# Kernel optimization log

Hardware: AMD Instinct MI355X
Metric: run time of the kernel (lower is better)

Reference implementation:

```python
import jax, jax.numpy as jnp
import numpy as np


def setup_inputs() -> dict:
    key = jax.random.key(0)
    ks = jax.random.split(key, 7)
    C, IC, H, W, B = 512, 256, 64, 64, 8
    N = H * W
    return {
        "x": jax.random.normal(ks[0], (B, C, H, W), dtype=jnp.float32),
        "w_phi": jax.random.normal(ks[1], (IC, C), dtype=jnp.float32) * 0.02,
        "w_theta": jax.random.normal(ks[2], (IC, C), dtype=jnp.float32) * 0.02,
        "w_g": jax.random.normal(ks[3], (IC, C), dtype=jnp.float32) * 0.02,
        "w_mask": jax.random.normal(ks[4], (C, IC), dtype=jnp.float32) * 0.02,
        "pos_embedding": jax.random.normal(ks[5], (1, N, N), dtype=jnp.float32),
        "pos_embedding_decoder": jax.random.normal(ks[6], (1, IC, H, W), dtype=jnp.float32),
    }


def reference(x, w_phi, w_theta, w_g, w_mask, pos_embedding, pos_embedding_decoder):
    b, c, h, w = x.shape
    n = h * w
    xf = x.reshape(b, c, n)  # [b, c, n]
    # 1x1 convs as channel matmuls
    phi = jnp.einsum('oc,bcn->bon', w_phi, xf)      # [b, ic, n]
    theta = jnp.einsum('oc,bcn->bon', w_theta, xf)  # [b, ic, n]
    g = jnp.einsum('oc,bcn->bon', w_g, xf) + pos_embedding_decoder.reshape(1, -1, n)
    g = jnp.swapaxes(g, 1, 2)  # [b, n, ic]
    # attention logits: theta^T @ phi -> [b, n_theta, n_phi], plus learned pos bias
    attn = jnp.einsum('bci,bcj->bij', theta, phi) + pos_embedding
    # NOTE: original softmax is over dim=1 (the theta/query axis), non-standard
    attn = jax.nn.softmax(attn, axis=1)
    y = jnp.einsum('bij,bjc->bic', attn, g)  # [b, n, ic]
    y = jnp.swapaxes(y, 1, 2).reshape(b, -1, n)  # [b, ic, n]
    mask = jnp.einsum('oc,bcn->bon', w_mask, y).reshape(b, c, h, w)
    return mask + x
```

## Files before the change

kernel.cpp:

```cpp
#include <hip/hip_runtime.h>

typedef short bf8 __attribute__((ext_vector_type(8)));
typedef float f32x4 __attribute__((ext_vector_type(4)));
typedef unsigned short us4 __attribute__((ext_vector_type(4)));
typedef unsigned short us8 __attribute__((ext_vector_type(8)));

#define DEVI __device__ __forceinline__

constexpr int NB = 8, NC = 512, NIC = 256, NS = 4096;

constexpr size_t OFF_XT  = 0;
constexpr size_t OFF_TP  = 33554432;
constexpr size_t OFF_POS = 67108864;
constexpr size_t OFF_G   = 100663296;
constexpr size_t OFF_G2  = 117440512;
constexpr size_t OFF_Y   = 134217728;
constexpr size_t OFF_WTP = 150994944;
constexpr size_t OFF_WG  = 151519232;
constexpr size_t OFF_WM  = 151781376;
constexpr size_t OFF_SP  = 152043520;

DEVI unsigned short f2bf(float f){
  unsigned u = __float_as_uint(f);
  u += 0x7fffu + ((u >> 16) & 1u);
  return (unsigned short)(u >> 16);
}
DEVI float bf2f(unsigned short b){ return __uint_as_float(((unsigned)b) << 16); }

DEVI void gld16(const void* g, void* l){
  __builtin_amdgcn_global_load_lds((const __attribute__((address_space(1))) unsigned int*)g,
                                   (__attribute__((address_space(3))) unsigned int*)l, 16, 0, 0);
}

DEVI void stage128x32(unsigned short* dst, const unsigned short* src, int ld, int wid, int lane){
#pragma unroll
  for (int r = 0; r < 2; ++r){
    int instr = wid + r * 4;
    int row = instr * 16 + (lane >> 2);
    gld16(src + (size_t)row * ld + (lane & 3) * 8, dst + instr * 512);
  }
}

DEVI void zero44(f32x4 (&a)[4][4]){
  f32x4 z = {0.f, 0.f, 0.f, 0.f};
#pragma unroll
  for (int i = 0; i < 4; ++i)
#pragma unroll
    for (int j = 0; j < 4; ++j) a[i][j] = z;
}

template<int NK>
DEVI void gemm128(const unsigned short* Ag, int lda, const unsigned short* Bg, int ldb,
                  unsigned short (&Ab)[2][4096], unsigned short (&Bb)[2][4096],
                  f32x4 (&acc)[4][4], int wid, int lane)
{
  const int wr = wid >> 1, wc = wid & 1;
  stage128x32(Ab[0], Ag, lda, wid, lane);
  stage128x32(Bb[0], Bg, ldb, wid, lane);
  __syncthreads();
  for (int kk = 0; kk < NK; ++kk){
    int cur = kk & 1;
    if (kk + 1 < NK){
      stage128x32(Ab[cur ^ 1], Ag + (kk + 1) * 32, lda, wid, lane);
      stage128x32(Bb[cur ^ 1], Bg + (kk + 1) * 32, ldb, wid, lane);
    }
    bf8 a[4], b[4];
#pragma unroll
    for (int f = 0; f < 4; ++f){
      a[f] = *(const bf8*)&Ab[cur][(wr * 64 + f * 16 + (lane & 15)) * 32 + (lane >> 4) * 8];
      b[f] = *(const bf8*)&Bb[cur][(wc * 64 + f * 16 + (lane & 15)) * 32 + (lane >> 4) * 8];
    }
#pragma unroll
    for (int i = 0; i < 4; ++i)
#pragma unroll
      for (int j = 0; j < 4; ++j)
        acc[i][j] = __builtin_amdgcn_mfma_f32_16x16x32_bf16(a[i], b[j], acc[i][j], 0, 0, 0);
    __syncthreads();
  }
}


__global__ void k_prep(const float* wphi, const float* wtheta, const float* wgf, const float* wmf,
                       unsigned short* wtp, unsigned short* wgb, unsigned short* wmb){
  int idx = (blockIdx.x * 256 + threadIdx.x) * 4;
  const float* src; unsigned short* dst;
  if (idx < 131072)      { src = wphi + idx;            dst = wtp + idx; }
  else if (idx < 262144) { src = wtheta + (idx - 131072); dst = wtp + idx; }
  else if (idx < 393216) { src = wgf + (idx - 262144);  dst = wgb + (idx - 262144); }
  else                   { src = wmf + (idx - 393216);  dst = wmb + (idx - 393216); }
  f32x4 v = *(const f32x4*)src;
  us4 o;
#pragma unroll
  for (int r = 0; r < 4; ++r) o[r] = f2bf(v[r]);
  *(us4*)dst = o;
}

__global__ void k_pos(const float* pos, unsigned short* posb){
  size_t base = ((size_t)blockIdx.x * 256 + threadIdx.x) * 8;
  f32x4 v0 = *(const f32x4*)&pos[base];
  f32x4 v1 = *(const f32x4*)&pos[base + 4];
  us8 o;
#pragma unroll
  for (int r = 0; r < 4; ++r){ o[r] = f2bf(v0[r]); o[r + 4] = f2bf(v1[r]); }
  *(us8*)&posb[base] = o;
}

__global__ void k_xt(const float* x, unsigned short* xT){
  int b = blockIdx.z, ct = blockIdx.y, nt = blockIdx.x;
  __shared__ float t[64][65];
  int tid = threadIdx.x;
  int c0 = ct * 64, n0 = nt * 64;
  const float* xp = x + (size_t)b * NC * NS;
#pragma unroll
  for (int it = 0; it < 16; ++it){
    int idx = it * 256 + tid; int r = idx >> 6, cc = idx & 63;
    t[r][cc] = xp[(size_t)(c0 + r) * NS + n0 + cc];
  }
  __syncthreads();
  unsigned short* xo = xT + (size_t)b * NS * NC;
#pragma unroll
  for (int it = 0; it < 16; ++it){
    int idx = it * 256 + tid; int r = idx >> 6, cc = idx & 63;
    xo[(size_t)(n0 + r) * NC + c0 + cc] = f2bf(t[cc][r]);
  }
}


__global__ __launch_bounds__(256, 2) void k_tp(const unsigned short* wtp, const unsigned short* xT,
                                               unsigned short* tp){
  int b = blockIdx.z, ot = blockIdx.y, nt = blockIdx.x;
  int tid = threadIdx.x, wid = tid >> 6, lane = tid & 63, wr = wid >> 1, wc = wid & 1;
  __shared__ unsigned short Ab[2][4096], Bb[2][4096];
  f32x4 acc[4][4]; zero44(acc);
  gemm128<16>(wtp + (size_t)(ot * 128) * 512, 512,
              xT + ((size_t)b * NS + nt * 128) * 512, 512, Ab, Bb, acc, wid, lane);
  unsigned short* out = tp + (size_t)b * NS * 512;
#pragma unroll
  for (int fr = 0; fr < 4; ++fr)
#pragma unroll
    for (int fc = 0; fc < 4; ++fc){
      int o0 = ot * 128 + wr * 64 + fr * 16 + ((lane >> 4) << 2);
      int n  = nt * 128 + wc * 64 + fc * 16 + (lane & 15);
      us4 v;
#pragma unroll
      for (int r = 0; r < 4; ++r) v[r] = f2bf(acc[fr][fc][r]);
      *(us4*)&out[(size_t)n * 512 + o0] = v;
    }
}

__global__ __launch_bounds__(256, 2) void k_g(const unsigned short* xT, const unsigned short* wgb,
                                              const float* pdec, unsigned short* gb){
  int b = blockIdx.z, ot = blockIdx.y, nt = blockIdx.x;
  int tid = threadIdx.x, wid = tid >> 6, lane = tid & 63, wr = wid >> 1, wc = wid & 1;
  __shared__ unsigned short Ab[2][4096], Bb[2][4096];
  f32x4 acc[4][4]; zero44(acc);
  gemm128<16>(xT + ((size_t)b * NS + nt * 128) * 512, 512,
              wgb + (size_t)(ot * 128) * 512, 512, Ab, Bb, acc, wid, lane);
#pragma unroll
  for (int fr = 0; fr < 4; ++fr)
#pragma unroll
    for (int fc = 0; fc < 4; ++fc){
      int n0 = nt * 128 + wr * 64 + fr * 16 + ((lane >> 4) << 2);
      int o  = ot * 128 + wc * 64 + fc * 16 + (lane & 15);
      f32x4 pd = *(const f32x4*)&pdec[(size_t)o * NS + n0];
      us4 v;
#pragma unroll
      for (int r = 0; r < 4; ++r) v[r] = f2bf(acc[fr][fc][r] + pd[r]);
      *(us4*)&gb[((size_t)b * NIC + o) * NS + n0] = v;
    }
}

__global__ __launch_bounds__(256, 2) void k_stats(const unsigned short* tp, const unsigned short* posb,
                                                  float* sp){
  int b = blockIdx.z, ih = blockIdx.y, jt = blockIdx.x;
  int tid = threadIdx.x, wid = tid >> 6, lane = tid & 63, wr = wid >> 1, wc = wid & 1;
  __shared__ unsigned short Ab[2][4096], Bb[2][4096];
  __shared__ float sred[2][2][64];
  float sacc[4][4];
#pragma unroll
  for (int i = 0; i < 4; ++i)
#pragma unroll
    for (int j = 0; j < 4; ++j) sacc[i][j] = 0.f;
  const unsigned short* tpb = tp + (size_t)b * NS * 512;
  const unsigned short* Ag = tpb + (size_t)(jt * 128) * 512;
  for (int it8 = 0; it8 < 8; ++it8){
    int i0 = (ih * 8 + it8) * 128;
    const unsigned short* Bg = tpb + (size_t)i0 * 512 + 256;
    f32x4 acc[4][4]; zero44(acc);
    gemm128<8>(Ag, 512, Bg, 512, Ab, Bb, acc, wid, lane);
#pragma unroll
    for (int fr = 0; fr < 4; ++fr)
#pragma unroll
      for (int fc = 0; fc < 4; ++fc){
        int ig  = i0 + wc * 64 + fc * 16 + (lane & 15);
        int jg0 = jt * 128 + wr * 64 + fr * 16 + ((lane >> 4) << 2);
        us4 pv = *(const us4*)&posb[(size_t)ig * NS + jg0];
#pragma unroll
        for (int r = 0; r < 4; ++r)
          sacc[fr][r] += __expf(acc[fr][fc][r] + bf2f(pv[r]));
      }
  }
#pragma unroll
  for (int m = 1; m <= 8; m <<= 1)
#pragma unroll
    for (int fr = 0; fr < 4; ++fr)
#pragma unroll
      for (int r = 0; r < 4; ++r)
        sacc[fr][r] += __shfl_xor(sacc[fr][r], m, 64);
  if ((lane & 15) == 0){
#pragma unroll
    for (int fr = 0; fr < 4; ++fr)
#pragma unroll
      for (int r = 0; r < 4; ++r)
        sred[wr][wc][fr * 16 + ((lane >> 4) << 2) + r] = sacc[fr][r];
  }
  __syncthreads();
  if (tid < 128){
    int jl = tid;
    sp[((size_t)b * 4 + ih) * NS + jt * 128 + jl] = sred[jl >> 6][0][jl & 63] + sred[jl >> 6][1][jl & 63];
  }
}

__global__ void k_sg(const unsigned short* gb, const float* sp, unsigned short* g2){
  size_t base = ((size_t)blockIdx.x * 256 + threadIdx.x) * 8;
  int b = (int)(base / ((size_t)NIC * NS));
  int j0 = (int)(base % NS);
  const float* spb = sp + (size_t)b * 4 * NS + j0;
  us8 gv = *(const us8*)&gb[base];
  us8 o;
#pragma unroll
  for (int r = 0; r < 8; ++r){
    float s = spb[r] + spb[NS + r] + spb[2 * NS + r] + spb[3 * NS + r];
    o[r] = f2bf(bf2f(gv[r]) / s);
  }
  *(us8*)&g2[base] = o;
}

__global__ __launch_bounds__(256, 2) void k_y(const unsigned short* tp, const unsigned short* posb,
                                              const unsigned short* g2, unsigned short* yb){
  int b = blockIdx.y, i0 = blockIdx.x * 64;
  int tid = threadIdx.x, wid = tid >> 6, lane = tid & 63;
  __shared__ unsigned short Th[64 * 264];
  __shared__ unsigned short Aph[2][4096];
  __shared__ unsigned short El[64 * 136];
  const unsigned short* tpb = tp + (size_t)b * NS * 512;
#pragma unroll
  for (int t = 0; t < 8; ++t){
    int cid = t * 256 + tid; int row = cid >> 5, ch = cid & 31;
    *(us8*)&Th[row * 264 + ch * 8] = *(const us8*)&tpb[(size_t)(i0 + row) * 512 + 256 + ch * 8];
  }
  f32x4 yacc[4][4]; zero44(yacc);
  __syncthreads();
  const unsigned short* g2b = g2 + (size_t)b * NIC * NS;
  for (int jt = 0; jt < 32; ++jt){
    int j0 = jt * 128;
    f32x4 lacc[2][4];
    {
      f32x4 z = {0.f, 0.f, 0.f, 0.f};
#pragma unroll
      for (int i = 0; i < 2; ++i)
#pragma unroll
        for (int j = 0; j < 4; ++j) lacc[i][j] = z;
    }
    stage128x32(Aph[0], tpb + (size_t)j0 * 512, 512, wid, lane);
    __syncthreads();
    for (int kk = 0; kk < 8; ++kk){
      int cur = kk & 1;
      if (kk < 7) stage128x32(Aph[cur ^ 1], tpb + (size_t)j0 * 512 + (kk + 1) * 32, 512, wid, lane);
      bf8 a[2], bbf[4];
#pragma unroll
      for (int f = 0; f < 2; ++f)
        a[f] = *(const bf8*)&Aph[cur][(wid * 32 + f * 16 + (lane & 15)) * 32 + (lane >> 4) * 8];
#pragma unroll
      for (int f = 0; f < 4; ++f)
        bbf[f] = *(const bf8*)&Th[(f * 16 + (lane & 15)) * 264 + kk * 32 + (lane >> 4) * 8];
#pragma unroll
      for (int i = 0; i < 2; ++i)
#pragma unroll
        for (int j = 0; j < 4; ++j)
          lacc[i][j] = __builtin_amdgcn_mfma_f32_16x16x32_bf16(a[i], bbf[j], lacc[i][j], 0, 0, 0);
      __syncthreads();
    }
#pragma unroll
    for (int fr = 0; fr < 2; ++fr)
#pragma unroll
      for (int fc = 0; fc < 4; ++fc){
        int il  = fc * 16 + (lane & 15);
        int jl0 = wid * 32 + fr * 16 + ((lane >> 4) << 2);
        us4 pv = *(const us4*)&posb[(size_t)(i0 + il) * NS + j0 + jl0];
        us4 ev;
#pragma unroll
        for (int r = 0; r < 4; ++r)
          ev[r] = f2bf(__expf(lacc[fr][fc][r] + bf2f(pv[r])));
        *(us4*)&El[il * 136 + jl0] = ev;
      }
    __syncthreads();
#pragma unroll
    for (int jk = 0; jk < 4; ++jk){
      bf8 eb[4];
#pragma unroll
      for (int f = 0; f < 4; ++f)
        eb[f] = *(const bf8*)&El[(f * 16 + (lane & 15)) * 136 + jk * 32 + (lane >> 4) * 8];
#pragma unroll
      for (int cf = 0; cf < 4; ++cf){
        int c = wid * 64 + cf * 16 + (lane & 15);
        bf8 ga = *(const bf8*)&g2b[(size_t)c * NS + j0 + jk * 32 + (lane >> 4) * 8];
#pragma unroll
        for (int f = 0; f < 4; ++f)
          yacc[cf][f] = __builtin_amdgcn_mfma_f32_16x16x32_bf16(ga, eb[f], yacc[cf][f], 0, 0, 0);
      }
    }
    __syncthreads();
  }
  unsigned short* yo = yb + (size_t)b * NS * NIC;
#pragma unroll
  for (int cf = 0; cf < 4; ++cf)
#pragma unroll
    for (int f = 0; f < 4; ++f){
      int c0 = wid * 64 + cf * 16 + ((lane >> 4) << 2);
      int ig = i0 + f * 16 + (lane & 15);
      us4 v;
#pragma unroll
      for (int r = 0; r < 4; ++r) v[r] = f2bf(yacc[cf][f][r]);
      *(us4*)&yo[(size_t)ig * NIC + c0] = v;
    }
}

__global__ __launch_bounds__(256, 2) void k_out(const unsigned short* yb, const unsigned short* wmb,
                                                const float* xg, float* outg){
  int b = blockIdx.z, cot = blockIdx.y, nt = blockIdx.x;
  int tid = threadIdx.x, wid = tid >> 6, lane = tid & 63, wr = wid >> 1, wc = wid & 1;
  __shared__ unsigned short Ab[2][4096], Bb[2][4096];
  f32x4 acc[4][4]; zero44(acc);
  gemm128<8>(yb + ((size_t)b * NS + nt * 128) * 256, 256,
             wmb + (size_t)(cot * 128) * 256, 256, Ab, Bb, acc, wid, lane);
#pragma unroll
  for (int fr = 0; fr < 4; ++fr)
#pragma unroll
    for (int fc = 0; fc < 4; ++fc){
      int n0 = nt * 128 + wr * 64 + fr * 16 + ((lane >> 4) << 2);
      int co = cot * 128 + wc * 64 + fc * 16 + (lane & 15);
      f32x4 xv = *(const f32x4*)&xg[((size_t)b * NC + co) * NS + n0];
      f32x4 ov = acc[fr][fc] + xv;
      *(f32x4*)&outg[((size_t)b * NC + co) * NS + n0] = ov;
    }
}

extern "C" void kernel_launch(void* const* d_in, const int* in_sizes, int n_in,
                              void* d_out, int out_size, void* d_ws, size_t ws_size,
                              hipStream_t stream){
  const float* x      = (const float*)d_in[0];
  const float* wphi   = (const float*)d_in[1];
  const float* wtheta = (const float*)d_in[2];
  const float* wgf    = (const float*)d_in[3];
  const float* wmf    = (const float*)d_in[4];
  const float* pos    = (const float*)d_in[5];
  const float* pdec   = (const float*)d_in[6];
  float* outg = (float*)d_out;
  char* ws = (char*)d_ws;
  unsigned short* xT   = (unsigned short*)(ws + OFF_XT);
  unsigned short* tp   = (unsigned short*)(ws + OFF_TP);
  unsigned short* posb = (unsigned short*)(ws + OFF_POS);
  unsigned short* gb   = (unsigned short*)(ws + OFF_G);
  unsigned short* g2   = (unsigned short*)(ws + OFF_G2);
  unsigned short* yb   = (unsigned short*)(ws + OFF_Y);
  unsigned short* wtp  = (unsigned short*)(ws + OFF_WTP);
  unsigned short* wgb  = (unsigned short*)(ws + OFF_WG);
  unsigned short* wmb  = (unsigned short*)(ws + OFF_WM);
  float* sp = (float*)(ws + OFF_SP);

  k_prep<<<512, 256, 0, stream>>>(wphi, wtheta, wgf, wmf, wtp, wgb, wmb);
  k_pos<<<8192, 256, 0, stream>>>(pos, posb);
  k_xt<<<dim3(64, 8, 8), 256, 0, stream>>>(x, xT);
  k_tp<<<dim3(32, 4, 8), 256, 0, stream>>>(wtp, xT, tp);
  k_g<<<dim3(32, 2, 8), 256, 0, stream>>>(xT, wgb, pdec, gb);
  k_stats<<<dim3(32, 4, 8), 256, 0, stream>>>(tp, posb, sp);
  k_sg<<<4096, 256, 0, stream>>>(gb, sp, g2);
  k_y<<<dim3(64, 8), 256, 0, stream>>>(tp, posb, g2, yb);
  k_out<<<dim3(32, 4, 8), 256, 0, stream>>>(yb, wmb, x, outg);
}
```

Before: 583.2 us.

## Fold softmax normalization into attention kernel and use 8-wave blocks

Replaces the pass that rescales all of g by column sums with a tiny kernel computing reciprocal sums, applied to exp values inside k_y. k_y now uses 512 threads, with waves split 4x2 over j and i, so each wave holds a smaller accumulator tile. It also raises wave priority during the PV MFMA phase and drops the trailing barrier. This removes one full read and write of g and should improve latency hiding, but each block stages more per wave and the barrier removal may race on El between iterations.

```diff
diff --git a/kernel.cpp b/kernel.cpp
--- a/kernel.cpp
+++ b/kernel.cpp
@@ -13,7 +13,7 @@
 constexpr size_t OFF_TP  = 33554432;
 constexpr size_t OFF_POS = 67108864;
 constexpr size_t OFF_G   = 100663296;
-constexpr size_t OFF_G2  = 117440512;
+constexpr size_t OFF_RS  = 117440512;
 constexpr size_t OFF_Y   = 134217728;
 constexpr size_t OFF_WTP = 150994944;
 constexpr size_t OFF_WG  = 151519232;
@@ -39,6 +39,11 @@
     int row = instr * 16 + (lane >> 2);
     gld16(src + (size_t)row * ld + (lane & 3) * 8, dst + instr * 512);
   }
+}
+
+DEVI void stageA8(unsigned short* dst, const unsigned short* src, int ld, int wid, int lane){
+  int row = wid * 16 + (lane >> 2);
+  gld16(src + (size_t)row * ld + (lane & 3) * 8, dst + wid * 512);
 }
 
 DEVI void zero44(f32x4 (&a)[4][4]){
@@ -221,104 +226,108 @@
   }
 }
 
-__global__ void k_sg(const unsigned short* gb, const float* sp, unsigned short* g2){
-  size_t base = ((size_t)blockIdx.x * 256 + threadIdx.x) * 8;
-  int b = (int)(base / ((size_t)NIC * NS));
-  int j0 = (int)(base % NS);
-  const float* spb = sp + (size_t)b * 4 * NS + j0;
-  us8 gv = *(const us8*)&gb[base];
-  us8 o;
-#pragma unroll
-  for (int r = 0; r < 8; ++r){
-    float s = spb[r] + spb[NS + r] + spb[2 * NS + r] + spb[3 * NS + r];
-    o[r] = f2bf(bf2f(gv[r]) / s);
-  }
-  *(us8*)&g2[base] = o;
-}
-
-__global__ __launch_bounds__(256, 2) void k_y(const unsigned short* tp, const unsigned short* posb,
-                                              const unsigned short* g2, unsigned short* yb){
+__global__ void k_rs(const float* sp, float* rs){
+  int idx = blockIdx.x * 256 + threadIdx.x;
+  int b = idx >> 12, j = idx & 4095;
+  const float* spb = sp + (size_t)b * 4 * NS + j;
+  rs[idx] = 1.f / (spb[0] + spb[NS] + spb[2 * NS] + spb[3 * NS]);
+}
+
+__global__ __launch_bounds__(512, 4) void k_y(const unsigned short* tp, const unsigned short* posb,
+                                              const unsigned short* gb, const float* rs,
+                                              unsigned short* yb){
   int b = blockIdx.y, i0 = blockIdx.x * 64;
   int tid = threadIdx.x, wid = tid >> 6, lane = tid & 63;
+  int jw = wid & 3, iw = wid >> 2;
   __shared__ unsigned short Th[64 * 264];
-  __shared__ unsigned short Aph[2][4096];
+  __shared__ unsigned short Aph[2][128 * 32];
   __shared__ unsigned short El[64 * 136];
   const unsigned short* tpb = tp + (size_t)b * NS * 512;
 #pragma unroll
-  for (int t = 0; t < 8; ++t){
-    int cid = t * 256 + tid; int row = cid >> 5, ch = cid & 31;
+  for (int t = 0; t < 4; ++t){
+    int cid = t * 512 + tid; int row = cid >> 5, ch = cid & 31;
     *(us8*)&Th[row * 264 + ch * 8] = *(const us8*)&tpb[(size_t)(i0 + row) * 512 + 256 + ch * 8];
   }
-  f32x4 yacc[4][4]; zero44(yacc);
+  f32x4 yacc[4][2];
+  {
+    f32x4 z = {0.f, 0.f, 0.f, 0.f};
+#pragma unroll
+    for (int i = 0; i < 4; ++i)
+#pragma unroll
+      for (int j = 0; j < 2; ++j) yacc[i][j] = z;
+  }
   __syncthreads();
-  const unsigned short* g2b = g2 + (size_t)b * NIC * NS;
+  const unsigned short* gbb = gb + (size_t)b * NIC * NS;
+  const float* rsb = rs + (size_t)b * NS;
   for (int jt = 0; jt < 32; ++jt){
     int j0 = jt * 128;
-    f32x4 lacc[2][4];
+    f32x4 lacc[2][2];
     {
       f32x4 z = {0.f, 0.f, 0.f, 0.f};
 #pragma unroll
       for (int i = 0; i < 2; ++i)
 #pragma unroll
-        for (int j = 0; j < 4; ++j) lacc[i][j] = z;
-    }
-    stage128x32(Aph[0], tpb + (size_t)j0 * 512, 512, wid, lane);
+        for (int j = 0; j < 2; ++j) lacc[i][j] = z;
+    }
+    stageA8(Aph[0], tpb + (size_t)j0 * 512, 512, wid, lane);
     __syncthreads();
     for (int kk = 0; kk < 8; ++kk){
       int cur = kk & 1;
-      if (kk < 7) stage128x32(Aph[cur ^ 1], tpb + (size_t)j0 * 512 + (kk + 1) * 32, 512, wid, lane);
-      bf8 a[2], bbf[4];
+      if (kk < 7) stageA8(Aph[cur ^ 1], tpb + (size_t)j0 * 512 + (kk + 1) * 32, 512, wid, lane);
+      bf8 a[2], bbf[2];
 #pragma unroll
       for (int f = 0; f < 2; ++f)
-        a[f] = *(const bf8*)&Aph[cur][(wid * 32 + f * 16 + (lane & 15)) * 32 + (lane >> 4) * 8];
-#pragma unroll
-      for (int f = 0; f < 4; ++f)
-        bbf[f] = *(const bf8*)&Th[(f * 16 + (lane & 15)) * 264 + kk * 32 + (lane >> 4) * 8];
+        a[f] = *(const bf8*)&Aph[cur][(jw * 32 + f * 16 + (lane & 15)) * 32 + (lane >> 4) * 8];
+#pragma unroll
+      for (int f = 0; f < 2; ++f)
+        bbf[f] = *(const bf8*)&Th[(iw * 32 + f * 16 + (lane & 15)) * 264 + kk * 32 + (lane >> 4) * 8];
 #pragma unroll
       for (int i = 0; i < 2; ++i)
 #pragma unroll
-        for (int j = 0; j < 4; ++j)
+        for (int j = 0; j < 2; ++j)
           lacc[i][j] = __builtin_amdgcn_mfma_f32_16x16x32_bf16(a[i], bbf[j], lacc[i][j], 0, 0, 0);
       __syncthreads();
     }
 #pragma unroll
     for (int fr = 0; fr < 2; ++fr)
 #pragma unroll
-      for (int fc = 0; fc < 4; ++fc){
-        int il  = fc * 16 + (lane & 15);
-        int jl0 = wid * 32 + fr * 16 + ((lane >> 4) << 2);
+      for (int fc = 0; fc < 2; ++fc){
+        int il  = iw * 32 + fc * 16 + (lane & 15);
+        int jl0 = jw * 32 + fr * 16 + ((lane >> 4) << 2);
         us4 pv = *(const us4*)&posb[(size_t)(i0 + il) * NS + j0 + jl0];
+        f32x4 rv = *(const f32x4*)&rsb[j0 + jl0];
         us4 ev;
 #pragma unroll
         for (int r = 0; r < 4; ++r)
-          ev[r] = f2bf(__expf(lacc[fr][fc][r] + bf2f(pv[r])));
+          ev[r] = f2bf(__expf(lacc[fr][fc][r] + bf2f(pv[r])) * rv[r]);
         *(us4*)&El[il * 136 + jl0] = ev;
       }
     __syncthreads();
+    __builtin_amdgcn_s_setprio(1);
 #pragma unroll
     for (int jk = 0; jk < 4; ++jk){
-      bf8 eb[4];
-#pragma unroll
-      for (int f = 0; f < 4; ++f)
-        eb[f] = *(const bf8*)&El[(f * 16 + (lane & 15)) * 136 + jk * 32 + (lane >> 4) * 8];
+      bf8 eb[2];
+#pragma unroll
+      for (int f = 0; f < 2; ++f)
+        eb[f] = *(const bf8*)&El[(iw * 32 + f * 16 + (lane & 15)) * 136 + jk * 32 + (lane >> 4) * 8];
 #pragma unroll
       for (int cf = 0; cf < 4; ++cf){
-        int c = wid * 64 + cf * 16 + (lane & 15);
-        bf8 ga = *(const bf8*)&g2b[(size_t)c * NS + j0 + jk * 32 + (lane >> 4) * 8];
-#pragma unroll
-        for (int f = 0; f < 4; ++f)
+        int c = jw * 64 + cf * 16 + (lane & 15);
+        bf8 ga = *(const bf8*)&gbb[(size_t)c * NS + j0 + jk * 32 + (lane >> 4) * 8];
+#pragma unroll
+        for (int f = 0; f < 2; ++f)
           yacc[cf][f] = __builtin_amdgcn_mfma_f32_16x16x32_bf16(ga, eb[f], yacc[cf][f], 0, 0, 0);
       }
     }
-    __syncthreads();
+    __builtin_amdgcn_s_setprio(0);
   }
   unsigned short* yo = yb + (size_t)b * NS * NIC;
 #pragma unroll
   for (int cf = 0; cf < 4; ++cf)
 #pragma unroll
-    for (int f = 0; f < 4; ++f){
-      int c0 = wid * 64 + cf * 16 + ((lane >> 4) << 2);
-      int ig = i0 + f * 16 + (lane & 15);
+    for (int f = 0; f < 2; ++f){
+      int c0 = jw * 64 + cf * 16 + ((lane >> 4) << 2);
+      int ig = i0 + iw * 32 + f * 16 + (lane & 15);
       us4 v;
 #pragma unroll
       for (int r = 0; r < 4; ++r) v[r] = f2bf(yacc[cf][f][r]);
@@ -362,7 +371,7 @@
   unsigned short* tp   = (unsigned short*)(ws + OFF_TP);
   unsigned short* posb = (unsigned short*)(ws + OFF_POS);
   unsigned short* gb   = (unsigned short*)(ws + OFF_G);
-  unsigned short* g2   = (unsigned short*)(ws + OFF_G2);
+  float*          rsv  = (float*)(ws + OFF_RS);
   unsigned short* yb   = (unsigned short*)(ws + OFF_Y);
   unsigned short* wtp  = (unsigned short*)(ws + OFF_WTP);
   unsigned short* wgb  = (unsigned short*)(ws + OFF_WG);
@@ -375,7 +384,7 @@
   k_tp<<<dim3(32, 4, 8), 256, 0, stream>>>(wtp, xT, tp);
   k_g<<<dim3(32, 2, 8), 256, 0, stream>>>(xT, wgb, pdec, gb);
   k_stats<<<dim3(32, 4, 8), 256, 0, stream>>>(tp, posb, sp);
-  k_sg<<<4096, 256, 0, stream>>>(gb, sp, g2);
-  k_y<<<dim3(64, 8), 256, 0, stream>>>(tp, posb, g2, yb);
+  k_rs<<<128, 256, 0, stream>>>(sp, rsv);
+  k_y<<<dim3(64, 8), 512, 0, stream>>>(tp, posb, gb, rsv, yb);
   k_out<<<dim3(32, 4, 8), 256, 0, stream>>>(yb, wmb, x, outg);
 }
```

Measured after the change: 666.3 us. 14.3% more time.
